# Performance work log

Measured on AMD Instinct MI355X. Metric: run time of the kernel, lower is better.

Reference implementation:

```python
import jax, jax.numpy as jnp
import numpy as np

GROUPS = 8
EPS = 1e-5
PAD = 2  # kernel_size - 1 ('full' padding for stride-1 transposed conv)


def setup_inputs() -> dict:
    key = jax.random.key(0)
    k_x, k_w = jax.random.split(key)
    x = jax.random.normal(k_x, (16, 24, 24, 24, 64), dtype=jnp.float32)
    conv_kernel = jax.random.normal(k_w, (3, 3, 3, 64, 128), dtype=jnp.float32) * 0.05
    gn_scale = jnp.ones((128,), dtype=jnp.float32)
    gn_bias = jnp.zeros((128,), dtype=jnp.float32)
    return {"x": x, "conv_kernel": conv_kernel, "gn_scale": gn_scale, "gn_bias": gn_bias}


def reference(x, conv_kernel, gn_scale, gn_bias):
    # Stride-1 ConvTranspose3d == regular conv with spatially flipped kernel and 'full' padding.
    k_flipped = jnp.flip(conv_kernel, axis=(0, 1, 2))  # DHWIO
    y = jax.lax.conv_general_dilated(
        x, k_flipped,
        window_strides=(1, 1, 1),
        padding=[(PAD, PAD)] * 3,
        dimension_numbers=("NDHWC", "DHWIO", "NDHWC"),
    )  # [B, D+2, H+2, W+2, C_out]
    y = jax.nn.relu(y)
    B, D, H, W, C = y.shape
    yr = y.reshape(B, D, H, W, GROUPS, C // GROUPS)
    mean = jnp.mean(yr, axis=(1, 2, 3, 5), keepdims=True)
    var = jnp.var(yr, axis=(1, 2, 3, 5), keepdims=True)
    yn = ((yr - mean) * jax.lax.rsqrt(var + EPS)).reshape(B, D, H, W, C)
    return yn * gn_scale + gn_bias
```

## Files before the change

kernel.cpp:

```cpp
#include <hip/hip_runtime.h>

#define N_    16
#define DIN   24
#define DOUT  26
#define CIN   64
#define COUT  128
#define NGRP  8
#define EPS   1e-5f

#define STATS_OFF 0
#define KF_OFF    1280
#define Y16_OFF   1048576
#define Y16_BYTES ((size_t)N_ * DOUT * DOUT * DOUT * COUT * 2)
#define Y16_END   ((size_t)Y16_OFF + Y16_BYTES)

typedef _Float16 half8_t  __attribute__((ext_vector_type(8)));
typedef float    f32x16_t __attribute__((ext_vector_type(16)));

__global__ __launch_bounds__(256) void convert_k_kernel(
    const float* __restrict__ K, _Float16* __restrict__ Kf, float* __restrict__ stats)
{
    int t = blockIdx.x * 256 + threadIdx.x;
    if (blockIdx.x == 0 && threadIdx.x < N_ * NGRP * 2) stats[threadIdx.x] = 0.0f;
    if (t >= 27 * 4 * 4 * 64) return;
    const int lane = t & 63;
    const int nf   = (t >> 6) & 3;
    const int ckg  = (t >> 8) & 3;
    const int tap  = t >> 10;
    const int ci0  = ckg * 16 + (lane >> 5) * 8;
    const int co   = nf * 32 + (lane & 31);
    half8_t h;
    #pragma unroll
    for (int j = 0; j < 8; ++j)
        h[j] = (_Float16)K[(size_t)(tap * CIN + ci0 + j) * COUT + co];
    *(half8_t*)(Kf + (size_t)t * 8) = h;
}

__global__ __launch_bounds__(256, 3) void conv_mfma16_kernel(
    const float* __restrict__ x, const _Float16* __restrict__ Kf,
    _Float16* __restrict__ y16, float* __restrict__ stats)
{
    __shared__ __align__(16) _Float16 xs[18 * 28 * 40];
    __shared__ float gsum[NGRP], gsq[NGRP];

    const int bid = blockIdx.x;
    const int n   = bid / (DOUT * 7);
    const int rem = bid % (DOUT * 7);
    const int d   = rem / 7;
    const int hb  = (rem % 7) * 4;
    const int tid = threadIdx.x;

    if (tid < NGRP) { gsum[tid] = 0.0f; gsq[tid] = 0.0f; }

    const int lane = tid & 63;
    const int wv   = tid >> 6;
    const int col  = lane & 31;
    const int hi   = lane >> 5;

    int aofs[3];
    #pragma unroll
    for (int aw = 0; aw < 3; ++aw) {
        int sl = col - aw + 2; if (sl > 27) sl = 27;
        aofs[aw] = sl * 40 + hi * 8;
    }

    f32x16_t acc[4];
    #pragma unroll
    for (int q = 0; q < 4; ++q) acc[q] = (f32x16_t)(0.0f);

    const _Float16* Kfl = Kf + (size_t)lane * 8 + (size_t)wv * 512;

    for (int ph = 0; ph < 2; ++ph) {
        for (int c = tid; c < 2016; c += 256) {
            const int s    = c / 112;
            const int rr   = c % 112;
            const int slot = rr >> 2;
            const int ch   = rr & 3;
            const int dd = d - s / 6;
            const int hh = hb + (s % 6) - 2;
            const int w  = slot - 2;
            half8_t v = {};
            if (dd >= 0 && dd < DIN && hh >= 0 && hh < DIN && w >= 0 && w < DIN) {
                const float* src = x + ((size_t)(((n * DIN + dd) * DIN + hh) * DIN + w)) * CIN
                                     + ph * 32 + ch * 8;
                const float4 a = *(const float4*)(src);
                const float4 b = *(const float4*)(src + 4);
                v[0] = (_Float16)a.x; v[1] = (_Float16)a.y; v[2] = (_Float16)a.z; v[3] = (_Float16)a.w;
                v[4] = (_Float16)b.x; v[5] = (_Float16)b.y; v[6] = (_Float16)b.z; v[7] = (_Float16)b.w;
            }
            *(half8_t*)(xs + s * 1120 + slot * 40 + ch * 8) = v;
        }
        __syncthreads();

        for (int ad = 0; ad < 3; ++ad) {
            #pragma unroll
            for (int ah = 0; ah < 3; ++ah) {
                const int sb  = (ad * 6 - ah + 2) * 1120;
                const int tap = (ad * 3 + ah) * 3;
                #pragma unroll
                for (int aw = 0; aw < 3; ++aw) {
                    #pragma unroll
                    for (int ck = 0; ck < 2; ++ck) {
                        half8_t b = *(const half8_t*)(
                            Kfl + (size_t)(((tap + aw) * 4 + ph * 2 + ck) * 4) * 512);
                        #pragma unroll
                        for (int q = 0; q < 4; ++q) {
                            half8_t a = *(const half8_t*)(xs + sb + q * 1120 + aofs[aw] + ck * 16);
                            acc[q] = __builtin_amdgcn_mfma_f32_32x32x16_f16(a, b, acc[q], 0, 0, 0);
                        }
                    }
                }
            }
        }
        if (ph == 0) __syncthreads();
    }

    #pragma unroll
    for (int q = 0; q < 4; ++q) {
        const int hrow = hb + q;
        if (hrow >= DOUT) continue;
        const size_t rowbase = (((size_t)(n * DOUT + d)) * DOUT + hrow) * (DOUT * COUT);
        const int cout = wv * 32 + col;
        float ls = 0.f, lsq = 0.f;
        #pragma unroll
        for (int reg = 0; reg < 16; ++reg) {
            const int wout = (reg & 3) + 8 * (reg >> 2) + 4 * hi;
            float v = fmaxf(acc[q][reg], 0.0f);
            if (wout < DOUT) {
                y16[rowbase + (size_t)wout * COUT + cout] = (_Float16)v;
                ls += v; lsq += v * v;
            }
        }
        #pragma unroll
        for (int off = 1; off < 16; off <<= 1) {
            ls  += __shfl_xor(ls, off);
            lsq += __shfl_xor(lsq, off);
        }
        ls  += __shfl_xor(ls, 32);
        lsq += __shfl_xor(lsq, 32);
        if (lane == 0 || lane == 16) {
            const int g = wv * 2 + (col >> 4);
            atomicAdd(&gsum[g], ls);
            atomicAdd(&gsq[g], lsq);
        }
    }
    __syncthreads();
    if (tid < NGRP) {
        atomicAdd(&stats[(n * NGRP + tid) * 2 + 0], gsum[tid]);
        atomicAdd(&stats[(n * NGRP + tid) * 2 + 1], gsq[tid]);
    }
}

__global__ __launch_bounds__(256) void gn16_apply_kernel(
    const _Float16* __restrict__ y16, float* __restrict__ y,
    const float* __restrict__ stats,
    const float* __restrict__ scale, const float* __restrict__ bias)
{
    const int total8 = N_ * DOUT * DOUT * DOUT * (COUT / 8);
    int i = blockIdx.x * 256 + threadIdx.x;
    if (i >= total8) return;

    const int t  = i & 15;
    const int co = t * 8;
    const int g  = t >> 1;
    const int n  = i / (DOUT * DOUT * DOUT * (COUT / 8));

    const float s  = stats[(n * NGRP + g) * 2 + 0];
    const float sq = stats[(n * NGRP + g) * 2 + 1];
    const float invN = 1.0f / (float)(DOUT * DOUT * DOUT * (COUT / NGRP));
    const float mean = s * invN;
    const float rstd = rsqrtf(sq * invN - mean * mean + EPS);

    const half8_t h = *(const half8_t*)(y16 + (size_t)i * 8);
    const float4 sc0 = *(const float4*)(scale + co);
    const float4 sc1 = *(const float4*)(scale + co + 4);
    const float4 bi0 = *(const float4*)(bias + co);
    const float4 bi1 = *(const float4*)(bias + co + 4);

    float4 o0, o1;
    o0.x = ((float)h[0] - mean) * rstd * sc0.x + bi0.x;
    o0.y = ((float)h[1] - mean) * rstd * sc0.y + bi0.y;
    o0.z = ((float)h[2] - mean) * rstd * sc0.z + bi0.z;
    o0.w = ((float)h[3] - mean) * rstd * sc0.w + bi0.w;
    o1.x = ((float)h[4] - mean) * rstd * sc1.x + bi1.x;
    o1.y = ((float)h[5] - mean) * rstd * sc1.y + bi1.y;
    o1.z = ((float)h[6] - mean) * rstd * sc1.z + bi1.z;
    o1.w = ((float)h[7] - mean) * rstd * sc1.w + bi1.w;
    ((float4*)y)[(size_t)i * 2]     = o0;
    ((float4*)y)[(size_t)i * 2 + 1] = o1;
}

__global__ __launch_bounds__(256, 3) void conv_mfma_kernel(
    const float* __restrict__ x, const _Float16* __restrict__ Kf,
    float* __restrict__ y, float* __restrict__ stats)
{
    __shared__ __align__(16) _Float16 xs[18 * 28 * 40];
    __shared__ float gsum[NGRP], gsq[NGRP];

    const int bid = blockIdx.x;
    const int n   = bid / (DOUT * 7);
    const int rem = bid % (DOUT * 7);
    const int d   = rem / 7;
    const int hb  = (rem % 7) * 4;
    const int tid = threadIdx.x;

    if (tid < NGRP) { gsum[tid] = 0.0f; gsq[tid] = 0.0f; }

    const int lane = tid & 63;
    const int wv   = tid >> 6;
    const int col  = lane & 31;
    const int hi   = lane >> 5;

    int aofs[3];
    #pragma unroll
    for (int aw = 0; aw < 3; ++aw) {
        int sl = col - aw + 2; if (sl > 27) sl = 27;
        aofs[aw] = sl * 40 + hi * 8;
    }

    f32x16_t acc[4];
    #pragma unroll
    for (int q = 0; q < 4; ++q) acc[q] = (f32x16_t)(0.0f);

    const _Float16* Kfl = Kf + (size_t)lane * 8 + (size_t)wv * 512;

    for (int ph = 0; ph < 2; ++ph) {
        for (int c = tid; c < 2016; c += 256) {
            const int s    = c / 112;
            const int rr   = c % 112;
            const int slot = rr >> 2;
            const int ch   = rr & 3;
            const int dd = d - s / 6;
            const int hh = hb + (s % 6) - 2;
            const int w  = slot - 2;
            half8_t v = {};
            if (dd >= 0 && dd < DIN && hh >= 0 && hh < DIN && w >= 0 && w < DIN) {
                const float* src = x + ((size_t)(((n * DIN + dd) * DIN + hh) * DIN + w)) * CIN
                                     + ph * 32 + ch * 8;
                const float4 a = *(const float4*)(src);
                const float4 b = *(const float4*)(src + 4);
                v[0] = (_Float16)a.x; v[1] = (_Float16)a.y; v[2] = (_Float16)a.z; v[3] = (_Float16)a.w;
                v[4] = (_Float16)b.x; v[5] = (_Float16)b.y; v[6] = (_Float16)b.z; v[7] = (_Float16)b.w;
            }
            *(half8_t*)(xs + s * 1120 + slot * 40 + ch * 8) = v;
        }
        __syncthreads();

        for (int ad = 0; ad < 3; ++ad) {
            #pragma unroll
            for (int ah = 0; ah < 3; ++ah) {
                const int sb  = (ad * 6 - ah + 2) * 1120;
                const int tap = (ad * 3 + ah) * 3;
                #pragma unroll
                for (int aw = 0; aw < 3; ++aw) {
                    #pragma unroll
                    for (int ck = 0; ck < 2; ++ck) {
                        half8_t b = *(const half8_t*)(
                            Kfl + (size_t)(((tap + aw) * 4 + ph * 2 + ck) * 4) * 512);
                        #pragma unroll
                        for (int q = 0; q < 4; ++q) {
                            half8_t a = *(const half8_t*)(xs + sb + q * 1120 + aofs[aw] + ck * 16);
                            acc[q] = __builtin_amdgcn_mfma_f32_32x32x16_f16(a, b, acc[q], 0, 0, 0);
                        }
                    }
                }
            }
        }
        if (ph == 0) __syncthreads();
    }

    #pragma unroll
    for (int q = 0; q < 4; ++q) {
        const int hrow = hb + q;
        if (hrow >= DOUT) continue;
        const size_t rowbase = (((size_t)(n * DOUT + d)) * DOUT + hrow) * (DOUT * COUT);
        const int cout = wv * 32 + col;
        float ls = 0.f, lsq = 0.f;
        #pragma unroll
        for (int reg = 0; reg < 16; ++reg) {
            const int wout = (reg & 3) + 8 * (reg >> 2) + 4 * hi;
            float v = fmaxf(acc[q][reg], 0.0f);
            if (wout < DOUT) {
                y[rowbase + (size_t)wout * COUT + cout] = v;
                ls += v; lsq += v * v;
            }
        }
        #pragma unroll
        for (int off = 1; off < 16; off <<= 1) {
            ls  += __shfl_xor(ls, off);
            lsq += __shfl_xor(lsq, off);
        }
        ls  += __shfl_xor(ls, 32);
        lsq += __shfl_xor(lsq, 32);
        if (lane == 0 || lane == 16) {
            const int g = wv * 2 + (col >> 4);
            atomicAdd(&gsum[g], ls);
            atomicAdd(&gsq[g], lsq);
        }
    }
    __syncthreads();
    if (tid < NGRP) {
        atomicAdd(&stats[(n * NGRP + tid) * 2 + 0], gsum[tid]);
        atomicAdd(&stats[(n * NGRP + tid) * 2 + 1], gsq[tid]);
    }
}

__global__ __launch_bounds__(256) void gn_apply_kernel(
    float* __restrict__ y, const float* __restrict__ stats,
    const float* __restrict__ scale, const float* __restrict__ bias)
{
    const int total4 = N_ * DOUT * DOUT * DOUT * (COUT / 4);
    int i = blockIdx.x * 256 + threadIdx.x;
    if (i >= total4) return;

    const int t  = i & 31;
    const int co = t * 4;
    const int g  = t >> 2;
    const int n  = i / (DOUT * DOUT * DOUT * (COUT / 4));

    const float s  = stats[(n * NGRP + g) * 2 + 0];
    const float sq = stats[(n * NGRP + g) * 2 + 1];
    const float invN = 1.0f / (float)(DOUT * DOUT * DOUT * (COUT / NGRP));
    const float mean = s * invN;
    const float var  = sq * invN - mean * mean;
    const float rstd = rsqrtf(var + EPS);

    float4 v = ((float4*)y)[i];
    const float4 sc = *(const float4*)(scale + co);
    const float4 bi = *(const float4*)(bias + co);
    v.x = (v.x - mean) * rstd * sc.x + bi.x;
    v.y = (v.y - mean) * rstd * sc.y + bi.y;
    v.z = (v.z - mean) * rstd * sc.z + bi.z;
    v.w = (v.w - mean) * rstd * sc.w + bi.w;
    ((float4*)y)[i] = v;
}

extern "C" void kernel_launch(void* const* d_in, const int* in_sizes, int n_in,
                              void* d_out, int out_size, void* d_ws, size_t ws_size,
                              hipStream_t stream) {
    const float* x     = (const float*)d_in[0];
    const float* K     = (const float*)d_in[1];
    const float* scale = (const float*)d_in[2];
    const float* bias  = (const float*)d_in[3];
    float* y = (float*)d_out;

    float*    stats = (float*)((char*)d_ws + STATS_OFF);
    _Float16* Kf    = (_Float16*)((char*)d_ws + KF_OFF);
    _Float16* y16   = (_Float16*)((char*)d_ws + Y16_OFF);

    convert_k_kernel<<<108, 256, 0, stream>>>(K, Kf, stats);

    if (ws_size >= Y16_END) {
        conv_mfma16_kernel<<<N_ * DOUT * 7, 256, 0, stream>>>(x, Kf, y16, stats);
        const int total8 = N_ * DOUT * DOUT * DOUT * (COUT / 8);
        gn16_apply_kernel<<<(total8 + 255) / 256, 256, 0, stream>>>(y16, y, stats, scale, bias);
    } else {
        conv_mfma_kernel<<<N_ * DOUT * 7, 256, 0, stream>>>(x, Kf, y, stats);
        const int total4 = N_ * DOUT * DOUT * DOUT * (COUT / 4);
        gn_apply_kernel<<<(total4 + 255) / 256, 256, 0, stream>>>(y, stats, scale, bias);
    }
}
```

Before: 345.4 us.

## Prefetch second channel half into registers during first MFMA pass; widen GN apply

The fp16 conv kernel now computes the global source pointers for its input tile once, and loads the second 32-channel half of the input into registers before running the first MFMA pass. This lets that global load overlap with compute instead of stalling after the first pass, at the cost of extra registers (eight half8 vectors plus cached pointers), which may hurt occupancy under the 3-blocks launch bound. The GN apply kernel also processes 16 channels per thread instead of 8, halving thread count and the per-thread stats and normalization setup.

```diff
diff --git a/kernel.cpp b/kernel.cpp
--- a/kernel.cpp
+++ b/kernel.cpp
@@ -36,9 +36,186 @@
     *(half8_t*)(Kf + (size_t)t * 8) = h;
 }
 
+#define MFMA_PASS(PH)                                                          \
+    for (int ad = 0; ad < 3; ++ad) {                                           \
+        _Pragma("unroll")                                                      \
+        for (int ah = 0; ah < 3; ++ah) {                                       \
+            const int sb  = (ad * 6 - ah + 2) * 1120;                          \
+            const int tap = (ad * 3 + ah) * 3;                                 \
+            _Pragma("unroll")                                                  \
+            for (int aw = 0; aw < 3; ++aw) {                                   \
+                _Pragma("unroll")                                              \
+                for (int ck = 0; ck < 2; ++ck) {                               \
+                    half8_t b = *(const half8_t*)(                             \
+                        Kfl + (size_t)(((tap + aw) * 4 + (PH) * 2 + ck) * 4) * 512); \
+                    _Pragma("unroll")                                          \
+                    for (int q = 0; q < 4; ++q) {                              \
+                        half8_t a = *(const half8_t*)(xs + sb + q * 1120 + aofs[aw] + ck * 16); \
+                        acc[q] = __builtin_amdgcn_mfma_f32_32x32x16_f16(a, b, acc[q], 0, 0, 0);  \
+                    }}}}}
+
 __global__ __launch_bounds__(256, 3) void conv_mfma16_kernel(
     const float* __restrict__ x, const _Float16* __restrict__ Kf,
     _Float16* __restrict__ y16, float* __restrict__ stats)
+{
+    __shared__ __align__(16) _Float16 xs[20480];
+    __shared__ float gsum[NGRP], gsq[NGRP];
+
+    const int bid = blockIdx.x;
+    const int n   = bid / (DOUT * 7);
+    const int rem = bid % (DOUT * 7);
+    const int d   = rem / 7;
+    const int hb  = (rem % 7) * 4;
+    const int tid = threadIdx.x;
+
+    if (tid < NGRP) { gsum[tid] = 0.0f; gsq[tid] = 0.0f; }
+
+    const int lane = tid & 63;
+    const int wv   = tid >> 6;
+    const int col  = lane & 31;
+    const int hi   = lane >> 5;
+
+    int aofs[3];
+    #pragma unroll
+    for (int aw = 0; aw < 3; ++aw) {
+        int sl = col - aw + 2; if (sl > 27) sl = 27;
+        aofs[aw] = sl * 40 + hi * 8;
+    }
+
+    f32x16_t acc[4];
+    #pragma unroll
+    for (int q = 0; q < 4; ++q) acc[q] = (f32x16_t)(0.0f);
+
+    const _Float16* Kfl = Kf + (size_t)lane * 8 + (size_t)wv * 512;
+
+    const float* srcp[8];
+    int dsto[8];
+    #pragma unroll
+    for (int k = 0; k < 8; ++k) {
+        const int c    = tid + k * 256;
+        const int s    = c / 112;
+        const int rr   = c % 112;
+        const int slot = rr >> 2;
+        const int ch   = rr & 3;
+        const int dd = d - s / 6;
+        const int hh = hb + (s % 6) - 2;
+        const int w  = slot - 2;
+        const float* sp = nullptr;
+        if (dd >= 0 && dd < DIN && hh >= 0 && hh < DIN && w >= 0 && w < DIN)
+            sp = x + ((size_t)(((n * DIN + dd) * DIN + hh) * DIN + w)) * CIN + ch * 8;
+        srcp[k] = sp;
+        dsto[k] = s * 1120 + slot * 40 + ch * 8;
+        half8_t v = {};
+        if (sp) {
+            const float4 a = *(const float4*)(sp);
+            const float4 b2 = *(const float4*)(sp + 4);
+            v[0] = (_Float16)a.x;  v[1] = (_Float16)a.y;  v[2] = (_Float16)a.z;  v[3] = (_Float16)a.w;
+            v[4] = (_Float16)b2.x; v[5] = (_Float16)b2.y; v[6] = (_Float16)b2.z; v[7] = (_Float16)b2.w;
+        }
+        *(half8_t*)(xs + dsto[k]) = v;
+    }
+    __syncthreads();
+
+    half8_t h1v[8];
+    #pragma unroll
+    for (int k = 0; k < 8; ++k) {
+        half8_t v = {};
+        if (srcp[k]) {
+            const float4 a = *(const float4*)(srcp[k] + 32);
+            const float4 b2 = *(const float4*)(srcp[k] + 36);
+            v[0] = (_Float16)a.x;  v[1] = (_Float16)a.y;  v[2] = (_Float16)a.z;  v[3] = (_Float16)a.w;
+            v[4] = (_Float16)b2.x; v[5] = (_Float16)b2.y; v[6] = (_Float16)b2.z; v[7] = (_Float16)b2.w;
+        }
+        h1v[k] = v;
+    }
+
+    MFMA_PASS(0)
+    __syncthreads();
+
+    #pragma unroll
+    for (int k = 0; k < 8; ++k)
+        *(half8_t*)(xs + dsto[k]) = h1v[k];
+    __syncthreads();
+
+    MFMA_PASS(1)
+
+    #pragma unroll
+    for (int q = 0; q < 4; ++q) {
+        const int hrow = hb + q;
+        if (hrow >= DOUT) continue;
+        const size_t rowbase = (((size_t)(n * DOUT + d)) * DOUT + hrow) * (DOUT * COUT);
+        const int cout = wv * 32 + col;
+        float ls = 0.f, lsq = 0.f;
+        #pragma unroll
+        for (int reg = 0; reg < 16; ++reg) {
+            const int wout = (reg & 3) + 8 * (reg >> 2) + 4 * hi;
+            float v = fmaxf(acc[q][reg], 0.0f);
+            if (wout < DOUT) {
+                y16[rowbase + (size_t)wout * COUT + cout] = (_Float16)v;
+                ls += v; lsq += v * v;
+            }
+        }
+        #pragma unroll
+        for (int off = 1; off < 16; off <<= 1) {
+            ls  += __shfl_xor(ls, off);
+            lsq += __shfl_xor(lsq, off);
+        }
+        ls  += __shfl_xor(ls, 32);
+        lsq += __shfl_xor(lsq, 32);
+        if (lane == 0 || lane == 16) {
+            const int g = wv * 2 + (col >> 4);
+            atomicAdd(&gsum[g], ls);
+            atomicAdd(&gsq[g], lsq);
+        }
+    }
+    __syncthreads();
+    if (tid < NGRP) {
+        atomicAdd(&stats[(n * NGRP + tid) * 2 + 0], gsum[tid]);
+        atomicAdd(&stats[(n * NGRP + tid) * 2 + 1], gsq[tid]);
+    }
+}
+
+__global__ __launch_bounds__(256) void gn16_apply_kernel(
+    const _Float16* __restrict__ y16, float* __restrict__ y,
+    const float* __restrict__ stats,
+    const float* __restrict__ scale, const float* __restrict__ bias)
+{
+    const int total16 = N_ * DOUT * DOUT * DOUT * (COUT / 16);
+    int i = blockIdx.x * 256 + threadIdx.x;
+    if (i >= total16) return;
+
+    const int t  = i & 7;
+    const int co = t * 16;
+    const int g  = t;
+    const int n  = i / (DOUT * DOUT * DOUT * (COUT / 16));
+
+    const float s  = stats[(n * NGRP + g) * 2 + 0];
+    const float sq = stats[(n * NGRP + g) * 2 + 1];
+    const float invN = 1.0f / (float)(DOUT * DOUT * DOUT * (COUT / NGRP));
+    const float mean = s * invN;
+    const float rstd = rsqrtf(sq * invN - mean * mean + EPS);
+
+    const half8_t h0 = *(const half8_t*)(y16 + (size_t)i * 16);
+    const half8_t h1 = *(const half8_t*)(y16 + (size_t)i * 16 + 8);
+
+    #pragma unroll
+    for (int c4 = 0; c4 < 4; ++c4) {
+        const float4 sc = *(const float4*)(scale + co + c4 * 4);
+        const float4 bi = *(const float4*)(bias + co + c4 * 4);
+        float4 o;
+        const half8_t& h = (c4 < 2) ? h0 : h1;
+        const int b0 = (c4 & 1) * 4;
+        o.x = ((float)h[b0 + 0] - mean) * rstd * sc.x + bi.x;
+        o.y = ((float)h[b0 + 1] - mean) * rstd * sc.y + bi.y;
+        o.z = ((float)h[b0 + 2] - mean) * rstd * sc.z + bi.z;
+        o.w = ((float)h[b0 + 3] - mean) * rstd * sc.w + bi.w;
+        ((float4*)y)[(size_t)i * 4 + c4] = o;
+    }
+}
+
+__global__ __launch_bounds__(256, 3) void conv_mfma_kernel(
+    const float* __restrict__ x, const _Float16* __restrict__ Kf,
+    float* __restrict__ y, float* __restrict__ stats)
 {
     __shared__ __align__(16) _Float16 xs[18 * 28 * 40];
     __shared__ float gsum[NGRP], gsq[NGRP];
@@ -127,160 +304,6 @@
             const int wout = (reg & 3) + 8 * (reg >> 2) + 4 * hi;
             float v = fmaxf(acc[q][reg], 0.0f);
             if (wout < DOUT) {
-                y16[rowbase + (size_t)wout * COUT + cout] = (_Float16)v;
-                ls += v; lsq += v * v;
-            }
-        }
-        #pragma unroll
-        for (int off = 1; off < 16; off <<= 1) {
-            ls  += __shfl_xor(ls, off);
-            lsq += __shfl_xor(lsq, off);
-        }
-        ls  += __shfl_xor(ls, 32);
-        lsq += __shfl_xor(lsq, 32);
-        if (lane == 0 || lane == 16) {
-            const int g = wv * 2 + (col >> 4);
-            atomicAdd(&gsum[g], ls);
-            atomicAdd(&gsq[g], lsq);
-        }
-    }
-    __syncthreads();
-    if (tid < NGRP) {
-        atomicAdd(&stats[(n * NGRP + tid) * 2 + 0], gsum[tid]);
-        atomicAdd(&stats[(n * NGRP + tid) * 2 + 1], gsq[tid]);
-    }
-}
-
-__global__ __launch_bounds__(256) void gn16_apply_kernel(
-    const _Float16* __restrict__ y16, float* __restrict__ y,
-    const float* __restrict__ stats,
-    const float* __restrict__ scale, const float* __restrict__ bias)
-{
-    const int total8 = N_ * DOUT * DOUT * DOUT * (COUT / 8);
-    int i = blockIdx.x * 256 + threadIdx.x;
-    if (i >= total8) return;
-
-    const int t  = i & 15;
-    const int co = t * 8;
-    const int g  = t >> 1;
-    const int n  = i / (DOUT * DOUT * DOUT * (COUT / 8));
-
-    const float s  = stats[(n * NGRP + g) * 2 + 0];
-    const float sq = stats[(n * NGRP + g) * 2 + 1];
-    const float invN = 1.0f / (float)(DOUT * DOUT * DOUT * (COUT / NGRP));
-    const float mean = s * invN;
-    const float rstd = rsqrtf(sq * invN - mean * mean + EPS);
-
-    const half8_t h = *(const half8_t*)(y16 + (size_t)i * 8);
-    const float4 sc0 = *(const float4*)(scale + co);
-    const float4 sc1 = *(const float4*)(scale + co + 4);
-    const float4 bi0 = *(const float4*)(bias + co);
-    const float4 bi1 = *(const float4*)(bias + co + 4);
-
-    float4 o0, o1;
-    o0.x = ((float)h[0] - mean) * rstd * sc0.x + bi0.x;
-    o0.y = ((float)h[1] - mean) * rstd * sc0.y + bi0.y;
-    o0.z = ((float)h[2] - mean) * rstd * sc0.z + bi0.z;
-    o0.w = ((float)h[3] - mean) * rstd * sc0.w + bi0.w;
-    o1.x = ((float)h[4] - mean) * rstd * sc1.x + bi1.x;
-    o1.y = ((float)h[5] - mean) * rstd * sc1.y + bi1.y;
-    o1.z = ((float)h[6] - mean) * rstd * sc1.z + bi1.z;
-    o1.w = ((float)h[7] - mean) * rstd * sc1.w + bi1.w;
-    ((float4*)y)[(size_t)i * 2]     = o0;
-    ((float4*)y)[(size_t)i * 2 + 1] = o1;
-}
-
-__global__ __launch_bounds__(256, 3) void conv_mfma_kernel(
-    const float* __restrict__ x, const _Float16* __restrict__ Kf,
-    float* __restrict__ y, float* __restrict__ stats)
-{
-    __shared__ __align__(16) _Float16 xs[18 * 28 * 40];
-    __shared__ float gsum[NGRP], gsq[NGRP];
-
-    const int bid = blockIdx.x;
-    const int n   = bid / (DOUT * 7);
-    const int rem = bid % (DOUT * 7);
-    const int d   = rem / 7;
-    const int hb  = (rem % 7) * 4;
-    const int tid = threadIdx.x;
-
-    if (tid < NGRP) { gsum[tid] = 0.0f; gsq[tid] = 0.0f; }
-
-    const int lane = tid & 63;
-    const int wv   = tid >> 6;
-    const int col  = lane & 31;
-    const int hi   = lane >> 5;
-
-    int aofs[3];
-    #pragma unroll
-    for (int aw = 0; aw < 3; ++aw) {
-        int sl = col - aw + 2; if (sl > 27) sl = 27;
-        aofs[aw] = sl * 40 + hi * 8;
-    }
-
-    f32x16_t acc[4];
-    #pragma unroll
-    for (int q = 0; q < 4; ++q) acc[q] = (f32x16_t)(0.0f);
-
-    const _Float16* Kfl = Kf + (size_t)lane * 8 + (size_t)wv * 512;
-
-    for (int ph = 0; ph < 2; ++ph) {
-        for (int c = tid; c < 2016; c += 256) {
-            const int s    = c / 112;
-            const int rr   = c % 112;
-            const int slot = rr >> 2;
-            const int ch   = rr & 3;
-            const int dd = d - s / 6;
-            const int hh = hb + (s % 6) - 2;
-            const int w  = slot - 2;
-            half8_t v = {};
-            if (dd >= 0 && dd < DIN && hh >= 0 && hh < DIN && w >= 0 && w < DIN) {
-                const float* src = x + ((size_t)(((n * DIN + dd) * DIN + hh) * DIN + w)) * CIN
-                                     + ph * 32 + ch * 8;
-                const float4 a = *(const float4*)(src);
-                const float4 b = *(const float4*)(src + 4);
-                v[0] = (_Float16)a.x; v[1] = (_Float16)a.y; v[2] = (_Float16)a.z; v[3] = (_Float16)a.w;
-                v[4] = (_Float16)b.x; v[5] = (_Float16)b.y; v[6] = (_Float16)b.z; v[7] = (_Float16)b.w;
-            }
-            *(half8_t*)(xs + s * 1120 + slot * 40 + ch * 8) = v;
-        }
-        __syncthreads();
-
-        for (int ad = 0; ad < 3; ++ad) {
-            #pragma unroll
-            for (int ah = 0; ah < 3; ++ah) {
-                const int sb  = (ad * 6 - ah + 2) * 1120;
-                const int tap = (ad * 3 + ah) * 3;
-                #pragma unroll
-                for (int aw = 0; aw < 3; ++aw) {
-                    #pragma unroll
-                    for (int ck = 0; ck < 2; ++ck) {
-                        half8_t b = *(const half8_t*)(
-                            Kfl + (size_t)(((tap + aw) * 4 + ph * 2 + ck) * 4) * 512);
-                        #pragma unroll
-                        for (int q = 0; q < 4; ++q) {
-                            half8_t a = *(const half8_t*)(xs + sb + q * 1120 + aofs[aw] + ck * 16);
-                            acc[q] = __builtin_amdgcn_mfma_f32_32x32x16_f16(a, b, acc[q], 0, 0, 0);
-                        }
-                    }
-                }
-            }
-        }
-        if (ph == 0) __syncthreads();
-    }
-
-    #pragma unroll
-    for (int q = 0; q < 4; ++q) {
-        const int hrow = hb + q;
-        if (hrow >= DOUT) continue;
-        const size_t rowbase = (((size_t)(n * DOUT + d)) * DOUT + hrow) * (DOUT * COUT);
-        const int cout = wv * 32 + col;
-        float ls = 0.f, lsq = 0.f;
-        #pragma unroll
-        for (int reg = 0; reg < 16; ++reg) {
-            const int wout = (reg & 3) + 8 * (reg >> 2) + 4 * hi;
-            float v = fmaxf(acc[q][reg], 0.0f);
-            if (wout < DOUT) {
                 y[rowbase + (size_t)wout * COUT + cout] = v;
                 ls += v; lsq += v * v;
             }
@@ -352,8 +375,8 @@
 
     if (ws_size >= Y16_END) {
         conv_mfma16_kernel<<<N_ * DOUT * 7, 256, 0, stream>>>(x, Kf, y16, stats);
-        const int total8 = N_ * DOUT * DOUT * DOUT * (COUT / 8);
-        gn16_apply_kernel<<<(total8 + 255) / 256, 256, 0, stream>>>(y16, y, stats, scale, bias);
+        const int total16 = N_ * DOUT * DOUT * DOUT * (COUT / 16);
+        gn16_apply_kernel<<<(total16 + 255) / 256, 256, 0, stream>>>(y16, y, stats, scale, bias);
     } else {
         conv_mfma_kernel<<<N_ * DOUT * 7, 256, 0, stream>>>(x, Kf, y, stats);
         const int total4 = N_ * DOUT * DOUT * DOUT * (COUT / 4);
```

After: 408.5 us. +18.3%, slower.
